# Kernel tuning notes

Measured on AMD Instinct MI355X. Metric: run time of the kernel, lower is better.

The kernel has to match this reference:

```python
import jax, jax.numpy as jnp
import numpy as np

B, S, D, H = 4, 2048, 768, 12
DK = D // H


def setup_inputs() -> dict:
    key = jax.random.key(0)
    ks = jax.random.split(key, 12)
    s = 1.0 / np.sqrt(D)
    return {
        "query": jax.random.normal(ks[0], (B, S, D), jnp.float32),
        "key_": jax.random.normal(ks[1], (B, S, D), jnp.float32),
        "value": jax.random.normal(ks[2], (B, S, D), jnp.float32),
        "mask": jax.random.randint(ks[3], (B, S), 0, 2, jnp.int32),
        # nn.Linear weights are (out_features, in_features); y = x @ W.T + b
        "Wq": jax.random.normal(ks[4], (D, D), jnp.float32) * s,
        "bq": jnp.zeros((D,), jnp.float32),
        "Wk": jax.random.normal(ks[5], (D, D), jnp.float32) * s,
        "bk": jnp.zeros((D,), jnp.float32),
        "Wv": jax.random.normal(ks[6], (D, D), jnp.float32) * s,
        "bv": jnp.zeros((D,), jnp.float32),
        "Wo": jax.random.normal(ks[7], (D, D), jnp.float32) * s,
        "bo": jnp.zeros((D,), jnp.float32),
    }


def reference(query, key_, value, mask, Wq, bq, Wk, bk, Wv, bv, Wo, bo):
    b = query.shape[0]
    # QKV projections, split heads: (B, S, D) -> (B, H, S, DK)
    def proj(x, W, bia):
        y = x @ W.T + bia
        return y.reshape(b, -1, H, DK).transpose(0, 2, 1, 3)

    q = proj(query, Wq, bq)
    k = proj(key_, Wk, bk)
    v = proj(value, Wv, bv)

    # Scaled dot-product attention with full [B, H, S, S] score matrix
    scores = jnp.einsum("bhqd,bhkd->bhqk", q, k) / jnp.sqrt(jnp.float32(DK))
    # mask: (B, S) broadcast over heads and query positions; masked_fill(mask==0, -1e9)
    scores = jnp.where(mask[:, None, None, :] == 0, jnp.float32(-1e9), scores)
    attn = jax.nn.softmax(scores, axis=-1)
    x = jnp.einsum("bhqk,bhkd->bhqd", attn, v)  # (B, H, S, DK)

    # merge heads and output projection
    x = x.transpose(0, 2, 1, 3).reshape(b, -1, H * DK)
    return x @ Wo.T + bo
```

## Files before the change

### kernel.cpp

```cpp
#include <hip/hip_runtime.h>
#include <math.h>

#define B_  4
#define S_  2048
#define D_  768
#define H_  12
#define DK_ 64
#define M_  (B_ * S_)
#define NBH_ (B_ * H_)

typedef float f32x4 __attribute__((ext_vector_type(4)));
typedef float f32x16 __attribute__((ext_vector_type(16)));
typedef __bf16 bf16x8 __attribute__((ext_vector_type(8)));
typedef unsigned u32x4v __attribute__((ext_vector_type(4)));

#if __has_builtin(__builtin_amdgcn_exp2f)
#define EXP2(x) __builtin_amdgcn_exp2f(x)
#else
#define EXP2(x) exp2f(x)
#endif

static __device__ __forceinline__ unsigned short f2bf(float f) {
    unsigned u = __builtin_bit_cast(unsigned, f);
    u += 0x7fffu + ((u >> 16) & 1u);
    return (unsigned short)(u >> 16);
}

static __device__ __forceinline__ unsigned cvt_pk_bf16(float lo, float hi) {
    unsigned r;
    asm("v_cvt_pk_bf16_f32 %0, %1, %2" : "=v"(r) : "v"(lo), "v"(hi));
    return r;
}

static __device__ __forceinline__ void gload_lds16(const void* g, void* l) {
    __builtin_amdgcn_global_load_lds(
        (const __attribute__((address_space(1))) void*)g,
        (__attribute__((address_space(3))) void*)l, 16, 0, 0);
}

static __device__ __forceinline__ void proj_body(
    const float* __restrict__ X, const float* __restrict__ W,
    const float* __restrict__ bias, void* __restrict__ outp, const int mode,
    const float oscale)
{
    __shared__ __align__(16) unsigned short As[2][128 * 32];
    __shared__ __align__(16) unsigned short Bs[2][128 * 32];

    const int t  = threadIdx.x;
    const int l  = t & 63;
    const int w  = t >> 6;
    const int lr = l & 15;
    const int lg = l >> 4;
    const int wm = w >> 1;
    const int wn = w & 1;
    const int m0 = blockIdx.x * 128;
    const int n0 = blockIdx.y * 128;

    const int v0r = t >> 2,         v0s = t & 3;
    const int v1r = (t + 256) >> 2, v1s = (t + 256) & 3;
    const int off0 = v0r * 32 + ((v0s ^ ((v0r >> 1) & 3)) << 3);
    const int off1 = v1r * 32 + ((v1s ^ ((v1r >> 1) & 3)) << 3);
    const float* xg0 = X + (size_t)(m0 + v0r) * D_ + v0s * 8;
    const float* xg1 = X + (size_t)(m0 + v1r) * D_ + v1s * 8;
    const float* wg0 = W + (size_t)(n0 + v0r) * D_ + v0s * 8;
    const float* wg1 = W + (size_t)(n0 + v1r) * D_ + v1s * 8;

    float4 pxa, pxb, pxc, pxd, pwa, pwb, pwc, pwd;

#define PROJ_LOAD(K0) do { \
        pxa = *(const float4*)(xg0 + (K0)); pxb = *(const float4*)(xg0 + (K0) + 4); \
        pxc = *(const float4*)(xg1 + (K0)); pxd = *(const float4*)(xg1 + (K0) + 4); \
        pwa = *(const float4*)(wg0 + (K0)); pwb = *(const float4*)(wg0 + (K0) + 4); \
        pwc = *(const float4*)(wg1 + (K0)); pwd = *(const float4*)(wg1 + (K0) + 4); \
    } while (0)

#define PROJ_STORE(BUF) do { \
        u32x4v xa_, xb_, wa_, wb_; \
        xa_.x = cvt_pk_bf16(pxa.x, pxa.y); xa_.y = cvt_pk_bf16(pxa.z, pxa.w); \
        xa_.z = cvt_pk_bf16(pxb.x, pxb.y); xa_.w = cvt_pk_bf16(pxb.z, pxb.w); \
        xb_.x = cvt_pk_bf16(pxc.x, pxc.y); xb_.y = cvt_pk_bf16(pxc.z, pxc.w); \
        xb_.z = cvt_pk_bf16(pxd.x, pxd.y); xb_.w = cvt_pk_bf16(pxd.z, pxd.w); \
        wa_.x = cvt_pk_bf16(pwa.x, pwa.y); wa_.y = cvt_pk_bf16(pwa.z, pwa.w); \
        wa_.z = cvt_pk_bf16(pwb.x, pwb.y); wa_.w = cvt_pk_bf16(pwb.z, pwb.w); \
        wb_.x = cvt_pk_bf16(pwc.x, pwc.y); wb_.y = cvt_pk_bf16(pwc.z, pwc.w); \
        wb_.z = cvt_pk_bf16(pwd.x, pwd.y); wb_.w = cvt_pk_bf16(pwd.z, pwd.w); \
        *(u32x4v*)&As[BUF][off0] = xa_; \
        *(u32x4v*)&As[BUF][off1] = xb_; \
        *(u32x4v*)&Bs[BUF][off0] = wa_; \
        *(u32x4v*)&Bs[BUF][off1] = wb_; \
    } while (0)

    f32x4 acc[4][4];
#pragma unroll
    for (int mi = 0; mi < 4; mi++)
#pragma unroll
        for (int ni = 0; ni < 4; ni++) acc[mi][ni] = (f32x4){0.f, 0.f, 0.f, 0.f};

    const int fsw = (lr >> 1) & 3;

    PROJ_LOAD(0);
    PROJ_STORE(0);
    __syncthreads();

    for (int kt = 0; kt < 24; kt++) {
        const int cur = kt & 1;
        const bool more = (kt < 23);

        if (more) PROJ_LOAD((kt + 1) * 32);

        bf16x8 af[4], bfr[4];
#pragma unroll
        for (int mi = 0; mi < 4; mi++) {
            int row = wm * 64 + mi * 16 + lr;
            af[mi] = *(const bf16x8*)&As[cur][row * 32 + ((lg ^ fsw) << 3)];
        }
#pragma unroll
        for (int ni = 0; ni < 4; ni++) {
            int row = wn * 64 + ni * 16 + lr;
            bfr[ni] = *(const bf16x8*)&Bs[cur][row * 32 + ((lg ^ fsw) << 3)];
        }
#pragma unroll
        for (int mi = 0; mi < 4; mi++)
#pragma unroll
            for (int ni = 0; ni < 4; ni++)
                acc[mi][ni] = __builtin_amdgcn_mfma_f32_16x16x32_bf16(
                    af[mi], bfr[ni], acc[mi][ni], 0, 0, 0);

        if (more) PROJ_STORE(cur ^ 1);
        __syncthreads();
    }

#undef PROJ_LOAD
#undef PROJ_STORE

    const int mrow0 = m0 + wm * 64;
    const int ncol0 = n0 + wn * 64;
    if (mode == 1) {
        float* out = (float*)outp;
#pragma unroll
        for (int mi = 0; mi < 4; mi++)
#pragma unroll
            for (int ni = 0; ni < 4; ni++) {
                int n = ncol0 + ni * 16 + lr;
                float bv = bias[n];
#pragma unroll
                for (int j = 0; j < 4; j++) {
                    int m = mrow0 + mi * 16 + 4 * lg + j;
                    out[(size_t)m * D_ + n] = acc[mi][ni][j] + bv;
                }
            }
    } else if (mode == 2) {
        unsigned short* out = (unsigned short*)outp;
#pragma unroll
        for (int mi = 0; mi < 4; mi++)
#pragma unroll
            for (int ni = 0; ni < 4; ni++) {
                int n = ncol0 + ni * 16 + lr;
                int h = n >> 6, dk = n & 63;
                float bv = bias[n];
                int m = mrow0 + mi * 16 + 4 * lg;
                int b = m >> 11, s = m & (S_ - 1);
                int slotp = ((s >> 3) & 7) ^ (dk & 7);
                int ssw = (s & ~63) | (slotp << 3) | (s & 7);
                uint2 o;
                o.x = cvt_pk_bf16(acc[mi][ni][0] + bv, acc[mi][ni][1] + bv);
                o.y = cvt_pk_bf16(acc[mi][ni][2] + bv, acc[mi][ni][3] + bv);
                *(uint2*)&out[((size_t)(b * H_ + h) * DK_ + dk) * S_ + ssw] = o;
            }
    } else {
        unsigned short* out = (unsigned short*)outp;
#pragma unroll
        for (int mi = 0; mi < 4; mi++)
#pragma unroll
            for (int ni = 0; ni < 4; ni++) {
                int n = ncol0 + ni * 16 + lr;
                int h = n >> 6, dk = n & 63;
                float bv = bias[n];
#pragma unroll
                for (int j = 0; j < 4; j++) {
                    int m = mrow0 + mi * 16 + 4 * lg + j;
                    int b = m >> 11, s = m & (S_ - 1);
                    int dko = (mode == 3)
                        ? ((dk & 7) | ((((dk >> 3) ^ (s & 7))) << 3)) : dk;
                    out[((size_t)(b * H_ + h) * S_ + s) * DK_ + dko] =
                        f2bf((acc[mi][ni][j] + bv) * oscale);
                }
            }
    }
}

__global__ __launch_bounds__(256) void proj_qkv(
    const float* __restrict__ Xq, const float* __restrict__ Xk,
    const float* __restrict__ Xv,
    const float* __restrict__ Wq, const float* __restrict__ bq,
    const float* __restrict__ Wk, const float* __restrict__ bk,
    const float* __restrict__ Wv, const float* __restrict__ bv,
    unsigned short* __restrict__ Qb, unsigned short* __restrict__ Kb,
    unsigned short* __restrict__ VT)
{
    const int z = blockIdx.z;
    const float* X    = (z == 0) ? Xq : (z == 1) ? Xk : Xv;
    const float* W    = (z == 0) ? Wq : (z == 1) ? Wk : Wv;
    const float* bias = (z == 0) ? bq : (z == 1) ? bk : bv;
    void* out         = (z == 0) ? (void*)Qb : (z == 1) ? (void*)Kb : (void*)VT;
    const int mode    = (z == 0) ? 0 : (z == 1) ? 3 : 2;
    const float osc   = (z == 0) ? 0.18033688011112042f : 1.0f;
    proj_body(X, W, bias, out, mode, osc);
}

__global__ __launch_bounds__(256) void proj_mfma(
    const float* __restrict__ X, const float* __restrict__ W,
    const float* __restrict__ bias, void* __restrict__ outp, const int mode,
    const float oscale)
{
    proj_body(X, W, bias, outp, mode, oscale);
}

__global__ __launch_bounds__(256) void attn_mfma(
    const unsigned short* __restrict__ Qb, const unsigned short* __restrict__ Kb,
    const unsigned short* __restrict__ VTb, const int* __restrict__ mask,
    float* __restrict__ O)
{
    __shared__ __align__(16) unsigned short Ks[2][64 * 64];
    __shared__ __align__(16) unsigned short Vs[2][64 * 64];

    const int tid = threadIdx.x;
    const int w  = tid >> 6;
    const int l  = tid & 63;
    const int q  = l & 31;
    const int hl = l >> 5;

    const int bh = blockIdx.x % NBH_;
    const int qt = blockIdx.x / NBH_;
    const int b  = bh / H_;
    const int hh = bh - b * H_;
    const int q0 = qt * 128 + w * 32;

    const unsigned short* qp = Qb + ((size_t)bh * S_ + q0 + q) * DK_;
    bf16x8 qf[4];
#pragma unroll
    for (int c = 0; c < 4; c++)
        qf[c] = *(const bf16x8*)(qp + c * 16 + hl * 8);

    const unsigned qext_sel = (hl == 0) ? 0x00003F80u : 0u;
    const unsigned bias_sel = (hl == 0) ? 0x0000C480u : 0u;
    u32x4v qe; qe.x = qext_sel; qe.y = 0u; qe.z = 0u; qe.w = 0u;
    const bf16x8 qf_ext = __builtin_bit_cast(bf16x8, qe);
    u32x4v on; on.x = on.y = on.z = on.w = 0x3F803F80u;
    const bf16x8 vOnes = __builtin_bit_cast(bf16x8, on);

    f32x16 acc0, acc1, accl;
#pragma unroll
    for (int i = 0; i < 16; i++) { acc0[i] = 0.f; acc1[i] = 0.f; accl[i] = 0.f; }

    const unsigned short* kbase = Kb + (size_t)bh * S_ * DK_;
    const unsigned short* vbase = VTb + (size_t)bh * DK_ * S_;
    const int* mbase = mask + b * S_;

    const unsigned short* kdma = kbase + (16 * w) * DK_ + l * 8;
    const unsigned short* vdma0 = vbase + (size_t)(16 * w + (l >> 3)) * S_ + (l & 7) * 8;
    const unsigned short* vdma1 = vdma0 + (size_t)8 * S_;

#define STAGE_DMA(J0, NB) do { \
        gload_lds16(kdma + (size_t)(J0) * DK_,            &Ks[NB][(16 * w) * 64]); \
        gload_lds16(kdma + (size_t)(J0) * DK_ + 8 * DK_,  &Ks[NB][(16 * w + 8) * 64]); \
        gload_lds16(vdma0 + (J0),                         &Vs[NB][(16 * w) * 64]); \
        gload_lds16(vdma1 + (J0),                         &Vs[NB][(16 * w + 8) * 64]); \
    } while (0)

    STAGE_DMA(0, 0);
    __syncthreads();

    const int fsw = (q & 7) << 3;
    const int kr0o = q * 64;
    const int kr1o = (32 + q) * 64;

    for (int tt = 0; tt < 32; tt++) {
        const int j0  = tt * 64;
        const int cur = tt & 1;

        if (tt < 31) {
            if (cur) STAGE_DMA(j0 + 64, 0); else STAGE_DMA(j0 + 64, 1);
        }

        int mv0 = mbase[j0 + q];
        int mv1 = mbase[j0 + 32 + q];
        u32x4v bw0; bw0.x = (mv0 == 0) ? bias_sel : 0u; bw0.y = 0u; bw0.z = 0u; bw0.w = 0u;
        u32x4v bw1; bw1.x = (mv1 == 0) ? bias_sel : 0u; bw1.y = 0u; bw1.z = 0u; bw1.w = 0u;
        bf16x8 kExt0 = __builtin_bit_cast(bf16x8, bw0);
        bf16x8 kExt1 = __builtin_bit_cast(bf16x8, bw1);

        f32x16 s0, s1;
#pragma unroll
        for (int i = 0; i < 16; i++) { s0[i] = 0.f; s1[i] = 0.f; }
        __builtin_amdgcn_s_setprio(1);
        s0 = __builtin_amdgcn_mfma_f32_32x32x16_bf16(kExt0, qf_ext, s0, 0, 0, 0);
        s1 = __builtin_amdgcn_mfma_f32_32x32x16_bf16(kExt1, qf_ext, s1, 0, 0, 0);
#pragma unroll
        for (int c = 0; c < 4; c++) {
            bf16x8 k0 = *(const bf16x8*)&Ks[cur][kr0o + ((c * 16 + hl * 8) ^ fsw)];
            bf16x8 k1 = *(const bf16x8*)&Ks[cur][kr1o + ((c * 16 + hl * 8) ^ fsw)];
            s0 = __builtin_amdgcn_mfma_f32_32x32x16_bf16(k0, qf[c], s0, 0, 0, 0);
            s1 = __builtin_amdgcn_mfma_f32_32x32x16_bf16(k1, qf[c], s1, 0, 0, 0);
        }
        __builtin_amdgcn_s_setprio(0);

#pragma unroll
        for (int r = 0; r < 16; r++) s0[r] = EXP2(s0[r]);
#pragma unroll
        for (int r = 0; r < 16; r++) s1[r] = EXP2(s1[r]);

#define SVAL(CP, I) (((CP) >> 1) ? s1[I] : s0[I])
        bf16x8 pb[4];
#pragma unroll
        for (int cp = 0; cp < 4; cp++) {
            const int e0 = 8 * (cp & 1);
            unsigned lo0 = cvt_pk_bf16(SVAL(cp, e0 + 0), SVAL(cp, e0 + 1));
            unsigned hi0 = cvt_pk_bf16(SVAL(cp, e0 + 2), SVAL(cp, e0 + 3));
            unsigned lo1 = cvt_pk_bf16(SVAL(cp, e0 + 4), SVAL(cp, e0 + 5));
            unsigned hi1 = cvt_pk_bf16(SVAL(cp, e0 + 6), SVAL(cp, e0 + 7));
            asm("v_permlane32_swap_b32 %0, %1" : "+v"(lo0), "+v"(lo1));
            asm("v_permlane32_swap_b32 %0, %1" : "+v"(hi0), "+v"(hi1));
            u32x4v pw;
            pw.x = lo0; pw.y = hi0; pw.z = lo1; pw.w = hi1;
            pb[cp] = __builtin_bit_cast(bf16x8, pw);
        }
#undef SVAL

        __builtin_amdgcn_s_setprio(1);
#pragma unroll
        for (int cp = 0; cp < 4; cp++) {
            bf16x8 v0 = *(const bf16x8*)&Vs[cur][kr0o + ((cp * 16 + hl * 8) ^ fsw)];
            bf16x8 v1 = *(const bf16x8*)&Vs[cur][kr1o + ((cp * 16 + hl * 8) ^ fsw)];
            acc0 = __builtin_amdgcn_mfma_f32_32x32x16_bf16(v0, pb[cp], acc0, 0, 0, 0);
            acc1 = __builtin_amdgcn_mfma_f32_32x32x16_bf16(v1, pb[cp], acc1, 0, 0, 0);
            accl = __builtin_amdgcn_mfma_f32_32x32x16_bf16(vOnes, pb[cp], accl, 0, 0, 0);
        }
        __builtin_amdgcn_s_setprio(0);

        __syncthreads();
    }
#undef STAGE_DMA

    float inv = 1.f / accl[0];
    float* ob = O + ((size_t)b * S_ + q0 + q) * D_ + hh * DK_;
#pragma unroll
    for (int b2 = 0; b2 < 4; b2++) {
        float4 o;
        o.x = acc0[4 * b2 + 0] * inv;
        o.y = acc0[4 * b2 + 1] * inv;
        o.z = acc0[4 * b2 + 2] * inv;
        o.w = acc0[4 * b2 + 3] * inv;
        *(float4*)(ob + 8 * b2 + 4 * hl) = o;
    }
#pragma unroll
    for (int b2 = 0; b2 < 4; b2++) {
        float4 o;
        o.x = acc1[4 * b2 + 0] * inv;
        o.y = acc1[4 * b2 + 1] * inv;
        o.z = acc1[4 * b2 + 2] * inv;
        o.w = acc1[4 * b2 + 3] * inv;
        *(float4*)(ob + 32 + 8 * b2 + 4 * hl) = o;
    }
}

extern "C" void kernel_launch(void* const* d_in, const int* in_sizes, int n_in,
                              void* d_out, int out_size, void* d_ws, size_t ws_size,
                              hipStream_t stream) {
    (void)in_sizes; (void)n_in; (void)out_size; (void)ws_size;

    const float* query = (const float*)d_in[0];
    const float* key_  = (const float*)d_in[1];
    const float* value = (const float*)d_in[2];
    const int*   mask  = (const int*)d_in[3];
    const float* Wq = (const float*)d_in[4];  const float* bq = (const float*)d_in[5];
    const float* Wk = (const float*)d_in[6];  const float* bk = (const float*)d_in[7];
    const float* Wv = (const float*)d_in[8];  const float* bv = (const float*)d_in[9];
    const float* Wo = (const float*)d_in[10]; const float* bo = (const float*)d_in[11];
    float* out = (float*)d_out;

    unsigned short* Qb = (unsigned short*)d_ws;
    unsigned short* Kb = Qb + (size_t)M_ * D_;
    unsigned short* VT = Kb + (size_t)M_ * D_;
    float*          Xb = (float*)(VT + (size_t)M_ * D_);

    dim3 gqkv(M_ / 128, D_ / 128, 3);
    proj_qkv<<<gqkv, 256, 0, stream>>>(query, key_, value,
                                       Wq, bq, Wk, bk, Wv, bv, Qb, Kb, VT);

    attn_mfma<<<dim3((S_ / 128) * NBH_), 256, 0, stream>>>(Qb, Kb, VT, mask, Xb);

    dim3 gproj(M_ / 128, D_ / 128);
    proj_mfma<<<gproj, 256, 0, stream>>>(Xb, Wo, bo, (void*)out, 1, 1.0f);
}
```

Baseline: 187.0 us.

## Pre-convert QKV inputs and weights to swizzled bf16 and load via global-to-LDS DMA

```diff
diff --git a/kernel.cpp b/kernel.cpp
--- a/kernel.cpp
+++ b/kernel.cpp
@@ -38,10 +38,185 @@
         (__attribute__((address_space(3))) void*)l, 16, 0, 0);
 }
 
-static __device__ __forceinline__ void proj_body(
-    const float* __restrict__ X, const float* __restrict__ W,
+__global__ __launch_bounds__(256) void cvt_x(
+    const float* __restrict__ q, const float* __restrict__ k,
+    const float* __restrict__ v,
+    unsigned short* __restrict__ q16, unsigned short* __restrict__ k16,
+    unsigned short* __restrict__ v16)
+{
+    const int z = blockIdx.y;
+    const float* src = (z == 0) ? q : (z == 1) ? k : v;
+    unsigned short* dst = (z == 0) ? q16 : (z == 1) ? k16 : v16;
+    const int NG = M_ * 96;
+    for (int g = blockIdx.x * 256 + threadIdx.x; g < NG; g += gridDim.x * 256) {
+        int r = g / 96, c8 = g - r * 96;
+        int kt = c8 >> 2, sl = c8 & 3;
+        const float* sp = src + (size_t)r * D_ + kt * 32 + sl * 8;
+        float4 a = *(const float4*)sp;
+        float4 b = *(const float4*)(sp + 4);
+        u32x4v o;
+        o.x = cvt_pk_bf16(a.x, a.y); o.y = cvt_pk_bf16(a.z, a.w);
+        o.z = cvt_pk_bf16(b.x, b.y); o.w = cvt_pk_bf16(b.z, b.w);
+        *(u32x4v*)(dst + (size_t)r * D_ + kt * 32 + ((sl ^ (r & 3)) << 3)) = o;
+    }
+}
+
+__global__ __launch_bounds__(256) void cvt_w(
+    const float* __restrict__ wq, const float* __restrict__ wk,
+    const float* __restrict__ wv,
+    unsigned short* __restrict__ wq16, unsigned short* __restrict__ wk16,
+    unsigned short* __restrict__ wv16)
+{
+    const int z = blockIdx.y;
+    const float* src = (z == 0) ? wq : (z == 1) ? wk : wv;
+    unsigned short* dst = (z == 0) ? wq16 : (z == 1) ? wk16 : wv16;
+    const int NG = D_ * 96;
+    for (int g = blockIdx.x * 256 + threadIdx.x; g < NG; g += gridDim.x * 256) {
+        int r = g / 96, c8 = g - r * 96;
+        int kt = c8 >> 2, sl = c8 & 3;
+        const float* sp = src + (size_t)r * D_ + kt * 32 + sl * 8;
+        float4 a = *(const float4*)sp;
+        float4 b = *(const float4*)(sp + 4);
+        u32x4v o;
+        o.x = cvt_pk_bf16(a.x, a.y); o.y = cvt_pk_bf16(a.z, a.w);
+        o.z = cvt_pk_bf16(b.x, b.y); o.w = cvt_pk_bf16(b.z, b.w);
+        *(u32x4v*)(dst + (size_t)r * D_ + kt * 32 + ((sl ^ (r & 3)) << 3)) = o;
+    }
+}
+
+static __device__ __forceinline__ void gemm_body_dma(
+    const unsigned short* __restrict__ A16, const unsigned short* __restrict__ B16,
     const float* __restrict__ bias, void* __restrict__ outp, const int mode,
     const float oscale)
+{
+    __shared__ __align__(16) unsigned short As[2][128 * 32];
+    __shared__ __align__(16) unsigned short Bs[2][128 * 32];
+
+    const int t  = threadIdx.x;
+    const int l  = t & 63;
+    const int w  = t >> 6;
+    const int lr = l & 15;
+    const int lg = l >> 4;
+    const int wm = w >> 1;
+    const int wn = w & 1;
+    const int m0 = blockIdx.x * 128;
+    const int n0 = blockIdx.y * 128;
+
+    const unsigned short* adma = A16 + (size_t)(m0 + 32 * w + (l >> 2)) * D_ + (l & 3) * 8;
+    const unsigned short* bdma = B16 + (size_t)(n0 + 32 * w + (l >> 2)) * D_ + (l & 3) * 8;
+
+#define GSTAGE(K0, NB) do { \
+        gload_lds16(adma + (K0),           &As[NB][(32 * w) * 32]); \
+        gload_lds16(adma + (K0) + 16 * D_, &As[NB][(32 * w + 16) * 32]); \
+        gload_lds16(bdma + (K0),           &Bs[NB][(32 * w) * 32]); \
+        gload_lds16(bdma + (K0) + 16 * D_, &Bs[NB][(32 * w + 16) * 32]); \
+    } while (0)
+
+    f32x4 acc[4][4];
+#pragma unroll
+    for (int mi = 0; mi < 4; mi++)
+#pragma unroll
+        for (int ni = 0; ni < 4; ni++) acc[mi][ni] = (f32x4){0.f, 0.f, 0.f, 0.f};
+
+    const int fsw = lr & 3;
+
+    GSTAGE(0, 0);
+    __syncthreads();
+
+    for (int kt = 0; kt < 24; kt++) {
+        const int cur = kt & 1;
+        if (kt < 23) {
+            if (cur) GSTAGE((kt + 1) * 32, 0);
+            else     GSTAGE((kt + 1) * 32, 1);
+        }
+
+        bf16x8 af[4], bfr[4];
+#pragma unroll
+        for (int mi = 0; mi < 4; mi++) {
+            int row = wm * 64 + mi * 16 + lr;
+            af[mi] = *(const bf16x8*)&As[cur][row * 32 + ((lg ^ fsw) << 3)];
+        }
+#pragma unroll
+        for (int ni = 0; ni < 4; ni++) {
+            int row = wn * 64 + ni * 16 + lr;
+            bfr[ni] = *(const bf16x8*)&Bs[cur][row * 32 + ((lg ^ fsw) << 3)];
+        }
+#pragma unroll
+        for (int mi = 0; mi < 4; mi++)
+#pragma unroll
+            for (int ni = 0; ni < 4; ni++)
+                acc[mi][ni] = __builtin_amdgcn_mfma_f32_16x16x32_bf16(
+                    af[mi], bfr[ni], acc[mi][ni], 0, 0, 0);
+
+        __syncthreads();
+    }
+#undef GSTAGE
+
+    const int mrow0 = m0 + wm * 64;
+    const int ncol0 = n0 + wn * 64;
+    if (mode == 2) {
+        unsigned short* out = (unsigned short*)outp;
+#pragma unroll
+        for (int mi = 0; mi < 4; mi++)
+#pragma unroll
+            for (int ni = 0; ni < 4; ni++) {
+                int n = ncol0 + ni * 16 + lr;
+                int h = n >> 6, dk = n & 63;
+                float bv = bias[n];
+                int m = mrow0 + mi * 16 + 4 * lg;
+                int b = m >> 11, s = m & (S_ - 1);
+                int slotp = ((s >> 3) & 7) ^ (dk & 7);
+                int ssw = (s & ~63) | (slotp << 3) | (s & 7);
+                uint2 o;
+                o.x = cvt_pk_bf16(acc[mi][ni][0] + bv, acc[mi][ni][1] + bv);
+                o.y = cvt_pk_bf16(acc[mi][ni][2] + bv, acc[mi][ni][3] + bv);
+                *(uint2*)&out[((size_t)(b * H_ + h) * DK_ + dk) * S_ + ssw] = o;
+            }
+    } else {
+        unsigned short* out = (unsigned short*)outp;
+#pragma unroll
+        for (int mi = 0; mi < 4; mi++)
+#pragma unroll
+            for (int ni = 0; ni < 4; ni++) {
+                int n = ncol0 + ni * 16 + lr;
+                int h = n >> 6, dk = n & 63;
+                float bv = bias[n];
+#pragma unroll
+                for (int j = 0; j < 4; j++) {
+                    int m = mrow0 + mi * 16 + 4 * lg + j;
+                    int b = m >> 11, s = m & (S_ - 1);
+                    int dko = (mode == 3)
+                        ? ((dk & 7) | ((((dk >> 3) ^ (s & 7))) << 3)) : dk;
+                    out[((size_t)(b * H_ + h) * S_ + s) * DK_ + dko] =
+                        f2bf((acc[mi][ni][j] + bv) * oscale);
+                }
+            }
+    }
+}
+
+__global__ __launch_bounds__(256) void gemm_qkv(
+    const unsigned short* __restrict__ q16, const unsigned short* __restrict__ k16,
+    const unsigned short* __restrict__ v16,
+    const unsigned short* __restrict__ wq16, const unsigned short* __restrict__ wk16,
+    const unsigned short* __restrict__ wv16,
+    const float* __restrict__ bq, const float* __restrict__ bk,
+    const float* __restrict__ bv,
+    unsigned short* __restrict__ Qb, unsigned short* __restrict__ Kb,
+    unsigned short* __restrict__ VT)
+{
+    const int z = blockIdx.z;
+    const unsigned short* A = (z == 0) ? q16 : (z == 1) ? k16 : v16;
+    const unsigned short* W = (z == 0) ? wq16 : (z == 1) ? wk16 : wv16;
+    const float* bias = (z == 0) ? bq : (z == 1) ? bk : bv;
+    void* out = (z == 0) ? (void*)Qb : (z == 1) ? (void*)Kb : (void*)VT;
+    const int mode = (z == 0) ? 0 : (z == 1) ? 3 : 2;
+    const float osc = (z == 0) ? 0.18033688011112042f : 1.0f;
+    gemm_body_dma(A, W, bias, out, mode, osc);
+}
+
+__global__ __launch_bounds__(256) void proj_mfma(
+    const float* __restrict__ X, const float* __restrict__ W,
+    const float* __restrict__ bias, float* __restrict__ out)
 {
     __shared__ __align__(16) unsigned short As[2][128 * 32];
     __shared__ __align__(16) unsigned short Bs[2][128 * 32];
@@ -135,85 +310,18 @@
 
     const int mrow0 = m0 + wm * 64;
     const int ncol0 = n0 + wn * 64;
-    if (mode == 1) {
-        float* out = (float*)outp;
-#pragma unroll
-        for (int mi = 0; mi < 4; mi++)
-#pragma unroll
-            for (int ni = 0; ni < 4; ni++) {
-                int n = ncol0 + ni * 16 + lr;
-                float bv = bias[n];
-#pragma unroll
-                for (int j = 0; j < 4; j++) {
-                    int m = mrow0 + mi * 16 + 4 * lg + j;
-                    out[(size_t)m * D_ + n] = acc[mi][ni][j] + bv;
-                }
+#pragma unroll
+    for (int mi = 0; mi < 4; mi++)
+#pragma unroll
+        for (int ni = 0; ni < 4; ni++) {
+            int n = ncol0 + ni * 16 + lr;
+            float bv = bias[n];
+#pragma unroll
+            for (int j = 0; j < 4; j++) {
+                int m = mrow0 + mi * 16 + 4 * lg + j;
+                out[(size_t)m * D_ + n] = acc[mi][ni][j] + bv;
             }
-    } else if (mode == 2) {
-        unsigned short* out = (unsigned short*)outp;
-#pragma unroll
-        for (int mi = 0; mi < 4; mi++)
-#pragma unroll
-            for (int ni = 0; ni < 4; ni++) {
-                int n = ncol0 + ni * 16 + lr;
-                int h = n >> 6, dk = n & 63;
-                float bv = bias[n];
-                int m = mrow0 + mi * 16 + 4 * lg;
-                int b = m >> 11, s = m & (S_ - 1);
-                int slotp = ((s >> 3) & 7) ^ (dk & 7);
-                int ssw = (s & ~63) | (slotp << 3) | (s & 7);
-                uint2 o;
-                o.x = cvt_pk_bf16(acc[mi][ni][0] + bv, acc[mi][ni][1] + bv);
-                o.y = cvt_pk_bf16(acc[mi][ni][2] + bv, acc[mi][ni][3] + bv);
-                *(uint2*)&out[((size_t)(b * H_ + h) * DK_ + dk) * S_ + ssw] = o;
-            }
-    } else {
-        unsigned short* out = (unsigned short*)outp;
-#pragma unroll
-        for (int mi = 0; mi < 4; mi++)
-#pragma unroll
-            for (int ni = 0; ni < 4; ni++) {
-                int n = ncol0 + ni * 16 + lr;
-                int h = n >> 6, dk = n & 63;
-                float bv = bias[n];
-#pragma unroll
-                for (int j = 0; j < 4; j++) {
-                    int m = mrow0 + mi * 16 + 4 * lg + j;
-                    int b = m >> 11, s = m & (S_ - 1);
-                    int dko = (mode == 3)
-                        ? ((dk & 7) | ((((dk >> 3) ^ (s & 7))) << 3)) : dk;
-                    out[((size_t)(b * H_ + h) * S_ + s) * DK_ + dko] =
-                        f2bf((acc[mi][ni][j] + bv) * oscale);
-                }
-            }
-    }
-}
-
-__global__ __launch_bounds__(256) void proj_qkv(
-    const float* __restrict__ Xq, const float* __restrict__ Xk,
-    const float* __restrict__ Xv,
-    const float* __restrict__ Wq, const float* __restrict__ bq,
-    const float* __restrict__ Wk, const float* __restrict__ bk,
-    const float* __restrict__ Wv, const float* __restrict__ bv,
-    unsigned short* __restrict__ Qb, unsigned short* __restrict__ Kb,
-    unsigned short* __restrict__ VT)
-{
-    const int z = blockIdx.z;
-    const float* X    = (z == 0) ? Xq : (z == 1) ? Xk : Xv;
-    const float* W    = (z == 0) ? Wq : (z == 1) ? Wk : Wv;
-    const float* bias = (z == 0) ? bq : (z == 1) ? bk : bv;
-    void* out         = (z == 0) ? (void*)Qb : (z == 1) ? (void*)Kb : (void*)VT;
-    const int mode    = (z == 0) ? 0 : (z == 1) ? 3 : 2;
-    const float osc   = (z == 0) ? 0.18033688011112042f : 1.0f;
-    proj_body(X, W, bias, out, mode, osc);
-}
-
-__global__ __launch_bounds__(256) void proj_mfma(
-    const float* __restrict__ X, const float* __restrict__ W,
-    const float* __restrict__ bias, void* __restrict__ outp, const int mode,
-    const float oscale)
-{
-    proj_body(X, W, bias, outp, mode, oscale);
+        }
 }
 
 __global__ __launch_bounds__(256) void attn_mfma(
@@ -379,17 +487,26 @@
     const float* Wo = (const float*)d_in[10]; const float* bo = (const float*)d_in[11];
     float* out = (float*)d_out;
 
-    unsigned short* Qb = (unsigned short*)d_ws;
-    unsigned short* Kb = Qb + (size_t)M_ * D_;
-    unsigned short* VT = Kb + (size_t)M_ * D_;
-    float*          Xb = (float*)(VT + (size_t)M_ * D_);
-
-    dim3 gqkv(M_ / 128, D_ / 128, 3);
-    proj_qkv<<<gqkv, 256, 0, stream>>>(query, key_, value,
-                                       Wq, bq, Wk, bk, Wv, bv, Qb, Kb, VT);
+    const size_t MD = (size_t)M_ * D_;
+    const size_t DD = (size_t)D_ * D_;
+    unsigned short* q16  = (unsigned short*)d_ws;
+    unsigned short* k16  = q16 + MD;
+    unsigned short* v16  = k16 + MD;
+    unsigned short* Qb   = v16 + MD;
+    unsigned short* Kb   = Qb + MD;
+    unsigned short* VT   = Kb + MD;
+    unsigned short* Wq16 = VT + MD;
+    unsigned short* Wk16 = Wq16 + DD;
+    unsigned short* Wv16 = Wk16 + DD;
+    float* Xb = (float*)q16;
+
+    cvt_x<<<dim3(1024, 3), 256, 0, stream>>>(query, key_, value, q16, k16, v16);
+    cvt_w<<<dim3(72, 3), 256, 0, stream>>>(Wq, Wk, Wv, Wq16, Wk16, Wv16);
+
+    gemm_qkv<<<dim3(M_ / 128, D_ / 128, 3), 256, 0, stream>>>(
+        q16, k16, v16, Wq16, Wk16, Wv16, bq, bk, bv, Qb, Kb, VT);
 
     attn_mfma<<<dim3((S_ / 128) * NBH_), 256, 0, stream>>>(Qb, Kb, VT, mask, Xb);
 
-    dim3 gproj(M_ / 128, D_ / 128);
-    proj_mfma<<<gproj, 256, 0, stream>>>(Xb, Wo, bo, (void*)out, 1, 1.0f);
-}
+    proj_mfma<<<dim3(M_ / 128, D_ / 128), 256, 0, stream>>>(Xb, Wo, bo, out);
+}
```

Result: slower. 199.6 us (+6.7%).
